# Kernel tuning notes

Measured on AMD Instinct MI355X. Metric: run time of the kernel, lower is better.

Reference implementation:

```python
import jax, jax.numpy as jnp
import numpy as np

N_HEAD, N_KV_HEAD, N_EMBD, SEQ_LEN = 16, 4, 1024, 2048
HEAD_DIM = N_EMBD // N_HEAD  # 64
B = 2


def _rope(x, cos, sin):
    # x: [B, T, H, D]; cos/sin: [1, T, 1, D//2]
    d = x.shape[-1] // 2
    x1, x2 = x[..., :d], x[..., d:]
    return jnp.concatenate([x1 * cos + x2 * sin, -x1 * sin + x2 * cos], axis=-1)


def setup_inputs() -> dict:
    key = jax.random.key(0)
    ks = jax.random.split(key, 5)
    x = jax.random.normal(ks[0], (B, SEQ_LEN, N_EMBD), dtype=jnp.float32)
    # real RoPE tables (base 10000)
    half = HEAD_DIM // 2
    inv_freq = 1.0 / (10000.0 ** (jnp.arange(half, dtype=jnp.float32) / half))
    ang = jnp.arange(SEQ_LEN, dtype=jnp.float32)[:, None] * inv_freq[None, :]  # [T, half]
    cos = jnp.cos(ang)[None, :, None, :]  # [1, T, 1, half]
    sin = jnp.sin(ang)[None, :, None, :]
    s = 0.02
    Wq = s * jax.random.normal(ks[1], (N_EMBD, N_HEAD * HEAD_DIM), dtype=jnp.float32)
    Wk = s * jax.random.normal(ks[2], (N_EMBD, N_KV_HEAD * HEAD_DIM), dtype=jnp.float32)
    Wv = s * jax.random.normal(ks[3], (N_EMBD, N_KV_HEAD * HEAD_DIM), dtype=jnp.float32)
    Wo = s * jax.random.normal(ks[4], (N_EMBD, N_EMBD), dtype=jnp.float32)
    return {"x": x, "cos": cos, "sin": sin, "Wq": Wq, "Wk": Wk, "Wv": Wv, "Wo": Wo}


def reference(x, cos, sin, Wq, Wk, Wv, Wo):
    Bsz, T, C = x.shape
    H, Hkv, D = N_HEAD, N_KV_HEAD, HEAD_DIM
    q = (x @ Wq).reshape(Bsz, T, H, D)
    k = (x @ Wk).reshape(Bsz, T, Hkv, D)
    v = (x @ Wv).reshape(Bsz, T, Hkv, D)
    q = _rope(q, cos, sin)
    k = _rope(k, cos, sin)
    # GQA: repeat kv heads to match query heads
    rep = H // Hkv
    k = jnp.repeat(k, rep, axis=2)  # [B, T, H, D]
    v = jnp.repeat(v, rep, axis=2)
    scale = 1.0 / np.sqrt(D).astype(np.float32)
    att = jnp.einsum('bqhd,bkhd->bhqk', q, k) * scale  # [B, H, T, T]
    causal = jnp.tril(jnp.ones((T, T), dtype=bool))
    att = jnp.where(causal[None, None, :, :], att, -jnp.inf)
    att = jax.nn.softmax(att, axis=-1)
    y = jnp.einsum('bhqk,bkhd->bqhd', att, v).reshape(Bsz, T, C)
    return y @ Wo
```

## Files before the change

kernel.cpp:

```cpp
#include <hip/hip_runtime.h>
#include <hip/hip_bf16.h>


typedef __attribute__((ext_vector_type(8))) short s16x8;
typedef __attribute__((ext_vector_type(16))) float f32x16;
typedef __attribute__((ext_vector_type(4))) float f32x4;
typedef __attribute__((ext_vector_type(4))) unsigned short u16x4;
typedef __attribute__((ext_vector_type(4))) unsigned int u32x4;

#define LOG2E 1.44269504088896340736f

__device__ __forceinline__ float bf2f(unsigned short u) {
  unsigned int i = ((unsigned int)u) << 16;
  return __builtin_bit_cast(float, i);
}
__device__ __forceinline__ unsigned short f2bf(float f) {
  unsigned int i = __builtin_bit_cast(unsigned int, f);
  i += 0x7fffu + ((i >> 16) & 1u);
  return (unsigned short)(i >> 16);
}
__device__ __forceinline__ unsigned int cvtpk(float lo, float hi) {
  unsigned int r;
  asm("v_cvt_pk_bf16_f32 %0, %1, %2" : "=v"(r) : "v"(lo), "v"(hi));
  return r;
}

__device__ __forceinline__ void async16(const void* g, void* l) {
  __builtin_amdgcn_global_load_lds(
      (const __attribute__((address_space(1))) void*)g,
      (__attribute__((address_space(3))) void*)l, 16, 0, 0);
}


__global__ void conv_f32_to_bf16(const float* __restrict__ in,
                                 unsigned short* __restrict__ out, int n) {
  int i = (blockIdx.x * blockDim.x + threadIdx.x) * 4;
  if (i + 3 < n) {
    float4 v = *(const float4*)(in + i);
    u16x4 o = { f2bf(v.x), f2bf(v.y), f2bf(v.z), f2bf(v.w) };
    *(u16x4*)(out + i) = o;
  }
}

__global__ void transpose_conv(const float* __restrict__ W,
                               unsigned short* __restrict__ Wt, int K, int N) {
  __shared__ float tile[32][33];
  int n0 = blockIdx.x * 32, k0 = blockIdx.y * 32;
  int tx = threadIdx.x, ty = threadIdx.y;
  for (int i = ty; i < 32; i += 8)
    tile[i][tx] = W[(size_t)(k0 + i) * N + n0 + tx];
  __syncthreads();
  for (int i = ty; i < 32; i += 8)
    Wt[(size_t)(n0 + i) * K + k0 + tx] = f2bf(tile[tx][i]);
}

__global__ void rope_qk(unsigned short* __restrict__ QKV,
                        const float* __restrict__ cosb,
                        const float* __restrict__ sinb) {
  int idx = blockIdx.x * blockDim.x + threadIdx.x;
  int d = idx & 31;
  int hh = (idx >> 5) % 20;
  int row = idx / (32 * 20);
  int t = row & 2047;
  size_t base;
  float mul;
  if (hh < 16) { base = (size_t)row * 1536 + hh * 64 + d;   mul = 0.125f * LOG2E; }
  else         { base = (size_t)row * 1536 + 1024 + (hh - 16) * 64 + d; mul = 1.0f; }
  float x1 = bf2f(QKV[base]), x2 = bf2f(QKV[base + 32]);
  float c = cosb[t * 32 + d], s = sinb[t * 32 + d];
  QKV[base]      = f2bf((x1 * c + x2 * s) * mul);
  QKV[base + 32] = f2bf((-x1 * s + x2 * c) * mul);
}

__global__ __launch_bounds__(256) void gemm_bt(
    const unsigned short* __restrict__ A, const unsigned short* __restrict__ Bt,
    void* __restrict__ Cp, int M, int N, int K, int c_f32) {
  __shared__ unsigned short As[128 * 64];
  __shared__ unsigned short Bs[64 * 64];
  int tid = threadIdx.x;
  int w = tid >> 6, l = tid & 63, g = l >> 4, lr = l & 15;
  int wr = w >> 1, wc = w & 1;
  int m0 = blockIdx.y * 128, n0 = blockIdx.x * 64;
  int sk = lr & 7;

  f32x4 acc[4][2] = {};

  for (int k0 = 0; k0 < K; k0 += 64) {
#pragma unroll
    for (int i = 0; i < 4; ++i) {
      int c = i * 256 + tid;
      int row = c >> 3, srcu = ((c & 7) ^ (row & 7)) * 8;
      async16(A + (size_t)(m0 + row) * K + k0 + srcu, (char*)As + c * 16);
    }
#pragma unroll
    for (int i = 0; i < 2; ++i) {
      int c = i * 256 + tid;
      int row = c >> 3, srcu = ((c & 7) ^ (row & 7)) * 8;
      async16(Bt + (size_t)(n0 + row) * K + k0 + srcu, (char*)Bs + c * 16);
    }
    __syncthreads();

    s16x8 af[2][4], bfr[2][2];
#pragma unroll
    for (int ks = 0; ks < 2; ++ks) {
#pragma unroll
      for (int m = 0; m < 4; ++m)
        af[ks][m] = *(const s16x8*)(As + (wr * 64 + m * 16 + lr) * 64 +
                                    ((ks * 4 + g) ^ sk) * 8);
#pragma unroll
      for (int n = 0; n < 2; ++n)
        bfr[ks][n] = *(const s16x8*)(Bs + (wc * 32 + n * 16 + lr) * 64 +
                                     ((ks * 4 + g) ^ sk) * 8);
    }
#pragma unroll
    for (int ks = 0; ks < 2; ++ks)
#pragma unroll
      for (int m = 0; m < 4; ++m)
#pragma unroll
        for (int n = 0; n < 2; ++n)
          acc[m][n] = __builtin_amdgcn_mfma_f32_16x16x32_bf16(
              af[ks][m], bfr[ks][n], acc[m][n], 0, 0, 0);
    __syncthreads();
  }

  if (c_f32) {
    float* C = (float*)Cp;
#pragma unroll
    for (int m = 0; m < 4; ++m)
#pragma unroll
      for (int n = 0; n < 2; ++n)
#pragma unroll
        for (int r = 0; r < 4; ++r)
          C[(size_t)(m0 + wr * 64 + m * 16 + g * 4 + r) * N +
            n0 + wc * 32 + n * 16 + lr] = acc[m][n][r];
  } else {
    unsigned short* C = (unsigned short*)Cp;
#pragma unroll
    for (int m = 0; m < 4; ++m)
#pragma unroll
      for (int n = 0; n < 2; ++n)
#pragma unroll
        for (int r = 0; r < 4; ++r)
          C[(size_t)(m0 + wr * 64 + m * 16 + g * 4 + r) * N +
            n0 + wc * 32 + n * 16 + lr] = f2bf(acc[m][n][r]);
  }
}

__global__ __launch_bounds__(128) void attn_fused(
    const unsigned short* __restrict__ QKV, unsigned short* __restrict__ Y) {
  __shared__ unsigned short Kt[2][64 * 64];
  __shared__ unsigned short Vt[2][64 * 64];

  const int T = 2048, CS = 1536;
  int tid = threadIdx.x;
  int wv = tid >> 6, l = tid & 63;
  int lq = l & 31, hi = l >> 5;
  int n = blockIdx.x;
  int qt = 31 - (n >> 5);
  int bh = n & 31, b = bh >> 4, h = bh & 15, kvh = h >> 2;
  int sx = l & 7;
  int qw = qt * 64 + wv * 32;
  int q_mine = qw + lq;

  const unsigned short* Qp = QKV + (size_t)b * T * CS + h * 64;
  const unsigned short* Kp = QKV + (size_t)b * T * CS + 1024 + kvh * 64;
  const unsigned short* Vp = QKV + (size_t)b * T * CS + 1280 + kvh * 64;

  s16x8 qf[4];
#pragma unroll
  for (int ks = 0; ks < 4; ++ks)
    qf[ks] = *(const s16x8*)(Qp + (size_t)q_mine * CS + ks * 16 + hi * 8);

  f32x16 o0 = {}, o1 = {};
  float mrun = -1e30f, lrun = 0.f;

  int ntiles = qt + 1;
  int kvi = (tid & 15) * 4, dc = (tid >> 4) * 8;

#pragma unroll
  for (int i = 0; i < 4; ++i) {
    int c = i * 128 + tid;
    int row = c >> 3, srcu = ((c & 7) ^ (row & 7)) * 8;
    async16(Kp + (size_t)row * CS + srcu, (char*)(&Kt[0][0]) + c * 16);
  }
  {
    s16x8 v0 = *(const s16x8*)(Vp + (size_t)(kvi + 0) * CS + dc);
    s16x8 v1 = *(const s16x8*)(Vp + (size_t)(kvi + 1) * CS + dc);
    s16x8 v2 = *(const s16x8*)(Vp + (size_t)(kvi + 2) * CS + dc);
    s16x8 v3 = *(const s16x8*)(Vp + (size_t)(kvi + 3) * CS + dc);
#pragma unroll
    for (int j = 0; j < 8; ++j) {
      u16x4 pk = { (unsigned short)v0[j], (unsigned short)v1[j],
                   (unsigned short)v2[j], (unsigned short)v3[j] };
      *(u16x4*)(&Vt[0][0] + (dc + j) * 64 + (kvi ^ (j * 8))) = pk;
    }
  }
  __syncthreads();

  int cur = 0;
  for (int it = 0; it < ntiles; ++it) {
    int kv0 = it * 64;
    bool hasnext = (it + 1 < ntiles);

    s16x8 v0, v1, v2, v3;
    if (hasnext) {
      int kvn = kv0 + 64;
#pragma unroll
      for (int i = 0; i < 4; ++i) {
        int c = i * 128 + tid;
        int row = c >> 3, srcu = ((c & 7) ^ (row & 7)) * 8;
        async16(Kp + (size_t)(kvn + row) * CS + srcu,
                (char*)(&Kt[cur ^ 1][0]) + c * 16);
      }
      v0 = *(const s16x8*)(Vp + (size_t)(kvn + kvi + 0) * CS + dc);
      v1 = *(const s16x8*)(Vp + (size_t)(kvn + kvi + 1) * CS + dc);
      v2 = *(const s16x8*)(Vp + (size_t)(kvn + kvi + 2) * CS + dc);
      v3 = *(const s16x8*)(Vp + (size_t)(kvn + kvi + 3) * CS + dc);
    }

    const unsigned short* Kc = &Kt[cur][0];
    const unsigned short* Vc = &Vt[cur][0];

    f32x16 s0 = {}, s1 = {};
    __builtin_amdgcn_s_setprio(1);
#pragma unroll
    for (int ks = 0; ks < 4; ++ks) {
      int u = ((ks * 2 + hi) ^ sx) * 8;
      s16x8 kf0 = *(const s16x8*)(Kc + lq * 64 + u);
      s16x8 kf1 = *(const s16x8*)(Kc + (32 + lq) * 64 + u);
      s0 = __builtin_amdgcn_mfma_f32_32x32x16_bf16(kf0, qf[ks], s0, 0, 0, 0);
      s1 = __builtin_amdgcn_mfma_f32_32x32x16_bf16(kf1, qf[ks], s1, 0, 0, 0);
    }
    __builtin_amdgcn_s_setprio(0);

    if (it == ntiles - 1) {
#pragma unroll
      for (int r = 0; r < 16; ++r) {
        int kvg = kv0 + (r & 3) + 8 * (r >> 2) + 4 * hi;
        if (kvg > q_mine) s0[r] = -1e30f;
        if (kvg + 32 > q_mine) s1[r] = -1e30f;
      }
    }

    float mt = s0[0];
#pragma unroll
    for (int r = 1; r < 16; ++r) mt = fmaxf(mt, s0[r]);
#pragma unroll
    for (int r = 0; r < 16; ++r) mt = fmaxf(mt, s1[r]);
    mt = fmaxf(mt, __shfl_xor(mt, 32, 64));

    if (__any(mt > mrun + 11.5416f)) {
      float mnew = fmaxf(mrun, mt);
      float corr = exp2f(mrun - mnew);
      float psum = 0.f;
#pragma unroll
      for (int r = 0; r < 16; ++r) {
        float p0 = exp2f(s0[r] - mnew); s0[r] = p0; psum += p0;
        float p1 = exp2f(s1[r] - mnew); s1[r] = p1; psum += p1;
      }
      psum += __shfl_xor(psum, 32, 64);
      lrun = lrun * corr + psum;
      mrun = mnew;
#pragma unroll
      for (int r = 0; r < 16; ++r) { o0[r] *= corr; o1[r] *= corr; }
    } else {
      float psum = 0.f;
#pragma unroll
      for (int r = 0; r < 16; ++r) {
        float p0 = exp2f(s0[r] - mrun); s0[r] = p0; psum += p0;
        float p1 = exp2f(s1[r] - mrun); s1[r] = p1; psum += p1;
      }
      psum += __shfl_xor(psum, 32, 64);
      lrun += psum;
    }

    __builtin_amdgcn_s_setprio(1);
#pragma unroll
    for (int ks = 0; ks < 4; ++ks) {
      int rb = (ks & 1) * 8;
      const f32x16& sp = (ks < 2) ? s0 : s1;
      unsigned int X0 = cvtpk(sp[rb + 0], sp[rb + 1]);
      unsigned int X1 = cvtpk(sp[rb + 2], sp[rb + 3]);
      unsigned int Y0 = cvtpk(sp[rb + 4], sp[rb + 5]);
      unsigned int Y1 = cvtpk(sp[rb + 6], sp[rb + 7]);
      unsigned int Z0 = hi ? X0 : Y0;
      unsigned int Z1 = hi ? X1 : Y1;
      unsigned int Zp0 = (unsigned int)__shfl_xor((int)Z0, 32, 64);
      unsigned int Zp1 = (unsigned int)__shfl_xor((int)Z1, 32, 64);
      u32x4 pw = { hi ? Zp0 : X0, hi ? Zp1 : X1,
                   hi ? Y0 : Zp0, hi ? Y1 : Zp1 };
      s16x8 pf = __builtin_bit_cast(s16x8, pw);
      int u = ((ks * 2 + hi) ^ sx) * 8;
      s16x8 vf0 = *(const s16x8*)(Vc + lq * 64 + u);
      s16x8 vf1 = *(const s16x8*)(Vc + (32 + lq) * 64 + u);
      o0 = __builtin_amdgcn_mfma_f32_32x32x16_bf16(vf0, pf, o0, 0, 0, 0);
      o1 = __builtin_amdgcn_mfma_f32_32x32x16_bf16(vf1, pf, o1, 0, 0, 0);
    }
    __builtin_amdgcn_s_setprio(0);

    if (hasnext) {
      unsigned short* Vn = &Vt[cur ^ 1][0];
#pragma unroll
      for (int j = 0; j < 8; ++j) {
        u16x4 pk = { (unsigned short)v0[j], (unsigned short)v1[j],
                     (unsigned short)v2[j], (unsigned short)v3[j] };
        *(u16x4*)(Vn + (dc + j) * 64 + (kvi ^ (j * 8))) = pk;
      }
    }
    __syncthreads();
    cur ^= 1;
  }

  float inv = 1.f / lrun;
  size_t rowoff = (size_t)(b * T + q_mine) * 1024 + h * 64;
#pragma unroll
  for (int rr = 0; rr < 4; ++rr) {
    int d0 = rr * 8 + 4 * hi;
    u16x4 w0 = { f2bf(o0[rr * 4 + 0] * inv), f2bf(o0[rr * 4 + 1] * inv),
                 f2bf(o0[rr * 4 + 2] * inv), f2bf(o0[rr * 4 + 3] * inv) };
    *(u16x4*)(Y + rowoff + d0) = w0;
    u16x4 w1 = { f2bf(o1[rr * 4 + 0] * inv), f2bf(o1[rr * 4 + 1] * inv),
                 f2bf(o1[rr * 4 + 2] * inv), f2bf(o1[rr * 4 + 3] * inv) };
    *(u16x4*)(Y + rowoff + 32 + d0) = w1;
  }
}


extern "C" void kernel_launch(void* const* d_in, const int* in_sizes, int n_in,
                              void* d_out, int out_size, void* d_ws, size_t ws_size,
                              hipStream_t stream) {
  const float* x    = (const float*)d_in[0];
  const float* cosb = (const float*)d_in[1];
  const float* sinb = (const float*)d_in[2];
  const float* Wq   = (const float*)d_in[3];
  const float* Wk   = (const float*)d_in[4];
  const float* Wv   = (const float*)d_in[5];
  const float* Wo   = (const float*)d_in[6];
  float* out = (float*)d_out;

  char* ob = (char*)d_out;
  char* ws = (char*)d_ws;
  const size_t MB = 1024 * 1024;
  unsigned short* QKVb  = (unsigned short*)(ob);
  unsigned short* xb    = (unsigned short*)(ws);
  unsigned short* Wqkvt = (unsigned short*)(ws + 8 * MB);
  unsigned short* Wot   = (unsigned short*)(ws + 11 * MB);
  unsigned short* Yb    = xb;

  conv_f32_to_bf16<<<4096, 256, 0, stream>>>(x, xb, 4096 * 1024);
  transpose_conv<<<dim3(32, 32), dim3(32, 8), 0, stream>>>(Wq, Wqkvt, 1024, 1024);
  transpose_conv<<<dim3(8, 32), dim3(32, 8), 0, stream>>>(Wk, Wqkvt + (size_t)1024 * 1024, 1024, 256);
  transpose_conv<<<dim3(8, 32), dim3(32, 8), 0, stream>>>(Wv, Wqkvt + (size_t)1280 * 1024, 1024, 256);
  transpose_conv<<<dim3(32, 32), dim3(32, 8), 0, stream>>>(Wo, Wot, 1024, 1024);

  gemm_bt<<<dim3(24, 32), 256, 0, stream>>>(xb, Wqkvt, QKVb, 4096, 1536, 1024, 0);

  rope_qk<<<10240, 256, 0, stream>>>(QKVb, cosb, sinb);

  attn_fused<<<dim3(1024), 128, 0, stream>>>(QKVb, Yb);

  gemm_bt<<<dim3(16, 32), 256, 0, stream>>>(Yb, Wot, out, 4096, 1024, 1024, 1);
}
```

Measured before the change: 142.9 us.

## Use single-wave attention blocks with K fragments loaded directly from global

The attention kernel now runs one 64-thread wave per block, each covering 32 query rows, so it launches twice as many blocks. K fragments are read straight from global memory into MFMA operand registers instead of being staged through a double-buffered LDS tile. V goes through a single LDS buffer, written each iteration from registers prefetched the previous iteration. This removes the block-wide __syncthreads and halves LDS use, aiming for higher occupancy and less synchronisation. The cost is that every wave now re-reads K and V from global or L2 on its own, with no reuse across waves, and K loads are less coalesced.

New measurement: 150.1 us. 5.1% more time.

```diff
diff --git a/kernel.cpp b/kernel.cpp
--- a/kernel.cpp
+++ b/kernel.cpp
@@ -146,21 +146,18 @@
   }
 }
 
-__global__ __launch_bounds__(128) void attn_fused(
+__global__ __launch_bounds__(64) void attn_fused(
     const unsigned short* __restrict__ QKV, unsigned short* __restrict__ Y) {
-  __shared__ unsigned short Kt[2][64 * 64];
-  __shared__ unsigned short Vt[2][64 * 64];
+  __shared__ unsigned short Vt[64 * 64];
 
   const int T = 2048, CS = 1536;
-  int tid = threadIdx.x;
-  int wv = tid >> 6, l = tid & 63;
+  int l = threadIdx.x;
   int lq = l & 31, hi = l >> 5;
   int n = blockIdx.x;
-  int qt = 31 - (n >> 5);
+  int qt = 63 - (n >> 5);
   int bh = n & 31, b = bh >> 4, h = bh & 15, kvh = h >> 2;
   int sx = l & 7;
-  int qw = qt * 64 + wv * 32;
-  int q_mine = qw + lq;
+  int q_mine = qt * 32 + lq;
 
   const unsigned short* Qp = QKV + (size_t)b * T * CS + h * 64;
   const unsigned short* Kp = QKV + (size_t)b * T * CS + 1024 + kvh * 64;
@@ -173,63 +170,54 @@
 
   f32x16 o0 = {}, o1 = {};
   float mrun = -1e30f, lrun = 0.f;
-
-  int ntiles = qt + 1;
-  int kvi = (tid & 15) * 4, dc = (tid >> 4) * 8;
-
-#pragma unroll
-  for (int i = 0; i < 4; ++i) {
-    int c = i * 128 + tid;
-    int row = c >> 3, srcu = ((c & 7) ^ (row & 7)) * 8;
-    async16(Kp + (size_t)row * CS + srcu, (char*)(&Kt[0][0]) + c * 16);
-  }
-  {
-    s16x8 v0 = *(const s16x8*)(Vp + (size_t)(kvi + 0) * CS + dc);
-    s16x8 v1 = *(const s16x8*)(Vp + (size_t)(kvi + 1) * CS + dc);
-    s16x8 v2 = *(const s16x8*)(Vp + (size_t)(kvi + 2) * CS + dc);
-    s16x8 v3 = *(const s16x8*)(Vp + (size_t)(kvi + 3) * CS + dc);
-#pragma unroll
-    for (int j = 0; j < 8; ++j) {
-      u16x4 pk = { (unsigned short)v0[j], (unsigned short)v1[j],
-                   (unsigned short)v2[j], (unsigned short)v3[j] };
-      *(u16x4*)(&Vt[0][0] + (dc + j) * 64 + (kvi ^ (j * 8))) = pk;
-    }
-  }
-  __syncthreads();
-
-  int cur = 0;
+  int ntiles = (qt >> 1) + 1;
+
+  int kvi = (l & 15) * 4, dc = (l >> 4) * 16;
+
+  s16x8 vv[8];
+#pragma unroll
+  for (int k4 = 0; k4 < 4; ++k4)
+#pragma unroll
+    for (int hf = 0; hf < 2; ++hf)
+      vv[k4 * 2 + hf] = *(const s16x8*)(Vp + (size_t)(kvi + k4) * CS + dc + hf * 8);
+
   for (int it = 0; it < ntiles; ++it) {
     int kv0 = it * 64;
     bool hasnext = (it + 1 < ntiles);
 
-    s16x8 v0, v1, v2, v3;
+    s16x8 kf0[4], kf1[4];
+#pragma unroll
+    for (int ks = 0; ks < 4; ++ks) {
+      kf0[ks] = *(const s16x8*)(Kp + (size_t)(kv0 + lq) * CS + ks * 16 + hi * 8);
+      kf1[ks] = *(const s16x8*)(Kp + (size_t)(kv0 + 32 + lq) * CS + ks * 16 + hi * 8);
+    }
+
+#pragma unroll
+    for (int hf = 0; hf < 2; ++hf)
+#pragma unroll
+      for (int j = 0; j < 8; ++j) {
+        int d = dc + hf * 8 + j;
+        u16x4 pk = { (unsigned short)vv[0 + hf][j], (unsigned short)vv[2 + hf][j],
+                     (unsigned short)vv[4 + hf][j], (unsigned short)vv[6 + hf][j] };
+        *(u16x4*)(&Vt[0] + d * 64 + (kvi ^ (j * 8))) = pk;
+      }
+
     if (hasnext) {
       int kvn = kv0 + 64;
 #pragma unroll
-      for (int i = 0; i < 4; ++i) {
-        int c = i * 128 + tid;
-        int row = c >> 3, srcu = ((c & 7) ^ (row & 7)) * 8;
-        async16(Kp + (size_t)(kvn + row) * CS + srcu,
-                (char*)(&Kt[cur ^ 1][0]) + c * 16);
-      }
-      v0 = *(const s16x8*)(Vp + (size_t)(kvn + kvi + 0) * CS + dc);
-      v1 = *(const s16x8*)(Vp + (size_t)(kvn + kvi + 1) * CS + dc);
-      v2 = *(const s16x8*)(Vp + (size_t)(kvn + kvi + 2) * CS + dc);
-      v3 = *(const s16x8*)(Vp + (size_t)(kvn + kvi + 3) * CS + dc);
-    }
-
-    const unsigned short* Kc = &Kt[cur][0];
-    const unsigned short* Vc = &Vt[cur][0];
+      for (int k4 = 0; k4 < 4; ++k4)
+#pragma unroll
+        for (int hf = 0; hf < 2; ++hf)
+          vv[k4 * 2 + hf] =
+              *(const s16x8*)(Vp + (size_t)(kvn + kvi + k4) * CS + dc + hf * 8);
+    }
 
     f32x16 s0 = {}, s1 = {};
     __builtin_amdgcn_s_setprio(1);
 #pragma unroll
     for (int ks = 0; ks < 4; ++ks) {
-      int u = ((ks * 2 + hi) ^ sx) * 8;
-      s16x8 kf0 = *(const s16x8*)(Kc + lq * 64 + u);
-      s16x8 kf1 = *(const s16x8*)(Kc + (32 + lq) * 64 + u);
-      s0 = __builtin_amdgcn_mfma_f32_32x32x16_bf16(kf0, qf[ks], s0, 0, 0, 0);
-      s1 = __builtin_amdgcn_mfma_f32_32x32x16_bf16(kf1, qf[ks], s1, 0, 0, 0);
+      s0 = __builtin_amdgcn_mfma_f32_32x32x16_bf16(kf0[ks], qf[ks], s0, 0, 0, 0);
+      s1 = __builtin_amdgcn_mfma_f32_32x32x16_bf16(kf1[ks], qf[ks], s1, 0, 0, 0);
     }
     __builtin_amdgcn_s_setprio(0);
 
@@ -291,24 +279,12 @@
                    hi ? Y0 : Zp0, hi ? Y1 : Zp1 };
       s16x8 pf = __builtin_bit_cast(s16x8, pw);
       int u = ((ks * 2 + hi) ^ sx) * 8;
-      s16x8 vf0 = *(const s16x8*)(Vc + lq * 64 + u);
-      s16x8 vf1 = *(const s16x8*)(Vc + (32 + lq) * 64 + u);
+      s16x8 vf0 = *(const s16x8*)(&Vt[0] + lq * 64 + u);
+      s16x8 vf1 = *(const s16x8*)(&Vt[0] + (32 + lq) * 64 + u);
       o0 = __builtin_amdgcn_mfma_f32_32x32x16_bf16(vf0, pf, o0, 0, 0, 0);
       o1 = __builtin_amdgcn_mfma_f32_32x32x16_bf16(vf1, pf, o1, 0, 0, 0);
     }
     __builtin_amdgcn_s_setprio(0);
-
-    if (hasnext) {
-      unsigned short* Vn = &Vt[cur ^ 1][0];
-#pragma unroll
-      for (int j = 0; j < 8; ++j) {
-        u16x4 pk = { (unsigned short)v0[j], (unsigned short)v1[j],
-                     (unsigned short)v2[j], (unsigned short)v3[j] };
-        *(u16x4*)(Vn + (dc + j) * 64 + (kvi ^ (j * 8))) = pk;
-      }
-    }
-    __syncthreads();
-    cur ^= 1;
   }
 
   float inv = 1.f / lrun;
@@ -357,7 +333,7 @@
 
   rope_qk<<<10240, 256, 0, stream>>>(QKVb, cosb, sinb);
 
-  attn_fused<<<dim3(1024), 128, 0, stream>>>(QKVb, Yb);
+  attn_fused<<<dim3(2048), 64, 0, stream>>>(QKVb, Yb);
 
   gemm_bt<<<dim3(16, 32), 256, 0, stream>>>(Yb, Wot, out, 4096, 1024, 1024, 1);
 }
```
